# Kernel tuning notes

Measured on AMD Instinct MI355X. Metric: run time of the kernel, lower is better.

The kernel has to match this reference:

```python
import jax, jax.numpy as jnp
import numpy as np

TEMPERATURE = 12.5   # args.temperature (DeepEMD default)
EPS = 0.05           # entropic regularization for the OT (EMD) solve
N_ITERS = 100        # Sinkhorn iterations
COS_EPS = 1e-8       # F.cosine_similarity eps


def setup_inputs() -> dict:
    key = jax.random.key(0)
    k1, k2 = jax.random.split(key)
    B, C, H, W = 512, 1024, 8, 8
    proto = jax.random.normal(k1, (B, C, H, W), dtype=jnp.float32)
    query = jax.random.normal(k2, (B, C, H, W), dtype=jnp.float32)
    return {"proto": proto, "query": query}


def get_weight_vector(A, Bmap):
    """A,[b,c,h,w]; pooled Bmap reweights A's channels -> node weights [b, h*w]."""
    pooled = Bmap.mean(axis=(2, 3), keepdims=True)          # adaptive_avg_pool2d -> [b,c,1,1]
    comb = (A * pooled).sum(axis=1).reshape(A.shape[0], -1)  # [b, h*w]
    return jax.nn.relu(comb) + 0.001


def center(x):
    # args.norm == 'center': subtract channel mean
    return x - x.mean(axis=1, keepdims=True)


def cosine_sim_map(proto, query):
    """sim[b, q_node, p_node] = cosine similarity between flattened spatial nodes."""
    B, C = proto.shape[0], proto.shape[1]
    p = proto.reshape(B, C, -1).transpose(0, 2, 1)   # [b, Np, c]
    q = query.reshape(B, C, -1).transpose(0, 2, 1)   # [b, Nq, c]
    pn = p / jnp.maximum(jnp.linalg.norm(p, axis=-1, keepdims=True), COS_EPS)
    qn = q / jnp.maximum(jnp.linalg.norm(q, axis=-1, keepdims=True), COS_EPS)
    return jnp.einsum('bqc,bpc->bqp', qn, pn)        # [b, Nq, Np]


def sinkhorn_flow(cost, r, c):
    """Entropic-regularized OT flow with marginals r [b,N], c [b,M]; cost [b,N,M]."""
    K = jnp.exp(-cost / EPS)
    v0 = jnp.ones_like(c)

    def body(v, _):
        u = r / jnp.maximum(jnp.einsum('bnm,bm->bn', K, v), 1e-30)
        v = c / jnp.maximum(jnp.einsum('bnm,bn->bm', K, u), 1e-30)
        return v, None

    v, _ = jax.lax.scan(body, v0, None, length=N_ITERS)
    u = r / jnp.maximum(jnp.einsum('bnm,bm->bn', K, v), 1e-30)
    return u[:, :, None] * K * v[:, None, :]         # [b, N, M]


def reference(proto, query):
    # emd_forward(proto, query)
    weight_1 = get_weight_vector(query, proto)       # [b, Nq]
    weight_2 = get_weight_vector(proto, query)       # [b, Np]
    p = center(proto)
    q = center(query)
    sim = cosine_sim_map(p, q)                       # [b, Nq, Np]
    # get_emd_distance: solve OT on cost = 1 - sim with (normalized) node weights
    r = weight_1 / weight_1.sum(axis=-1, keepdims=True)
    c = weight_2 / weight_2.sum(axis=-1, keepdims=True)
    flow = sinkhorn_flow(1.0 - sim, r, c)
    num_node = weight_1.shape[-1]
    logits = (sim * flow).sum(axis=(-1, -2)) * (TEMPERATURE / num_node)
    return logits
```

## Files before the change

### kernel.cpp

```cpp
#include <hip/hip_runtime.h>
#include <math.h>

#define NCH    1024
#define NN     64
#define CK     32
#define KSC    28.853900817779268f
#define SPLIT  4
#define WSB    4352

#define STAT_Q(v) { sqp[0]+=(v).x; q2p[0]=fmaf((v).x,(v).x,q2p[0]); \
                    sqp[1]+=(v).y; q2p[1]=fmaf((v).y,(v).y,q2p[1]); \
                    sqp[2]+=(v).z; q2p[2]=fmaf((v).z,(v).z,q2p[2]); \
                    sqp[3]+=(v).w; q2p[3]=fmaf((v).w,(v).w,q2p[3]); }
#define STAT_P(v) { spp[0]+=(v).x; p2p[0]=fmaf((v).x,(v).x,p2p[0]); \
                    spp[1]+=(v).y; p2p[1]=fmaf((v).y,(v).y,p2p[1]); \
                    spp[2]+=(v).z; p2p[2]=fmaf((v).z,(v).z,p2p[2]); \
                    spp[3]+=(v).w; p2p[3]=fmaf((v).w,(v).w,p2p[3]); }

#define GRAM_CHUNK_BODY(NCHUNK_, QB_, PB_)                                     \
    for (int ch = 0; ch < (NCHUNK_); ++ch) {                                   \
        if (ch) __syncthreads();                                               \
        *(float4*)&stage[       ofs] = qv0;                                    \
        *(float4*)&stage[1024 + ofs] = qv1;                                    \
        *(float4*)&stage[2048 + ofs] = pv0;                                    \
        *(float4*)&stage[3072 + ofs] = pv1;                                    \
        float4 nq0, nq1, np0, np1;                                             \
        const bool more = (ch + 1 < (NCHUNK_));                                \
        if (more) {                                                            \
            const float* qn = (QB_) + (ch + 1) * 2048;                         \
            const float* pn = (PB_) + (ch + 1) * 2048;                         \
            nq0 = *(const float4*)(qn + ofs);                                  \
            nq1 = *(const float4*)(qn + 1024 + ofs);                           \
            np0 = *(const float4*)(pn + ofs);                                  \
            np1 = *(const float4*)(pn + 1024 + ofs);                           \
        }                                                                      \
        STAT_Q(qv0); STAT_Q(qv1);                                              \
        STAT_P(pv0); STAT_P(pv1);                                              \
        __syncthreads();                                                       \
        _Pragma("unroll 8")                                                    \
        for (int cc = 0; cc < CK; ++cc) {                                      \
            float4 a  = *(const float4*)&stage[cc * 64 + n0];                  \
            float4 bb = *(const float4*)&stage[2048 + cc * 64 + m0];           \
            acc[0][0]=fmaf(a.x,bb.x,acc[0][0]); acc[0][1]=fmaf(a.x,bb.y,acc[0][1]); \
            acc[0][2]=fmaf(a.x,bb.z,acc[0][2]); acc[0][3]=fmaf(a.x,bb.w,acc[0][3]); \
            acc[1][0]=fmaf(a.y,bb.x,acc[1][0]); acc[1][1]=fmaf(a.y,bb.y,acc[1][1]); \
            acc[1][2]=fmaf(a.y,bb.z,acc[1][2]); acc[1][3]=fmaf(a.y,bb.w,acc[1][3]); \
            acc[2][0]=fmaf(a.z,bb.x,acc[2][0]); acc[2][1]=fmaf(a.z,bb.y,acc[2][1]); \
            acc[2][2]=fmaf(a.z,bb.z,acc[2][2]); acc[2][3]=fmaf(a.z,bb.w,acc[2][3]); \
            acc[3][0]=fmaf(a.w,bb.x,acc[3][0]); acc[3][1]=fmaf(a.w,bb.y,acc[3][1]); \
            acc[3][2]=fmaf(a.w,bb.z,acc[3][2]); acc[3][3]=fmaf(a.w,bb.w,acc[3][3]); \
        }                                                                      \
        if (more) { qv0 = nq0; qv1 = nq1; pv0 = np0; pv1 = np1; }              \
    }

#define DOT16(KK, ARR) ({ \
    float4 x0 = *(const float4*)&ARR[sp4*16 +  0]; \
    float4 x1 = *(const float4*)&ARR[sp4*16 +  4]; \
    float4 x2 = *(const float4*)&ARR[sp4*16 +  8]; \
    float4 x3 = *(const float4*)&ARR[sp4*16 + 12]; \
    float a0 = 0.0f, a1 = 0.0f; \
    a0=fmaf(KK[0],x0.x,a0);  a1=fmaf(KK[1],x0.y,a1); \
    a0=fmaf(KK[2],x0.z,a0);  a1=fmaf(KK[3],x0.w,a1); \
    a0=fmaf(KK[4],x1.x,a0);  a1=fmaf(KK[5],x1.y,a1); \
    a0=fmaf(KK[6],x1.z,a0);  a1=fmaf(KK[7],x1.w,a1); \
    a0=fmaf(KK[8],x2.x,a0);  a1=fmaf(KK[9],x2.y,a1); \
    a0=fmaf(KK[10],x2.z,a0); a1=fmaf(KK[11],x2.w,a1); \
    a0=fmaf(KK[12],x3.x,a0); a1=fmaf(KK[13],x3.y,a1); \
    a0=fmaf(KK[14],x3.z,a0); a1=fmaf(KK[15],x3.w,a1); \
    a0 + a1; })

__global__ __launch_bounds__(256)
void gram_partial(const float* __restrict__ proto,
                  const float* __restrict__ query,
                  float* __restrict__ ws)
{
    __shared__ __align__(16) float stage[4096];

    const int bid = blockIdx.x;
    const int b = bid >> 2, s = bid & (SPLIT - 1);
    const int t  = threadIdx.x;
    const int tr = t >> 4, tc = t & 15;
    const int n0 = tr * 4, m0 = tc * 4;
    const int ofs = 4 * t;

    const float* __restrict__ pb = proto + (size_t)b * (NCH * NN) + s * (NCH / SPLIT) * NN;
    const float* __restrict__ qb = query + (size_t)b * (NCH * NN) + s * (NCH / SPLIT) * NN;

    float acc[4][4];
    #pragma unroll
    for (int i = 0; i < 4; ++i)
        #pragma unroll
        for (int j = 0; j < 4; ++j) acc[i][j] = 0.0f;
    float sqp[4] = {0,0,0,0}, q2p[4] = {0,0,0,0};
    float spp[4] = {0,0,0,0}, p2p[4] = {0,0,0,0};

    float4 qv0 = *(const float4*)(qb + ofs);
    float4 qv1 = *(const float4*)(qb + 1024 + ofs);
    float4 pv0 = *(const float4*)(pb + ofs);
    float4 pv1 = *(const float4*)(pb + 1024 + ofs);

    GRAM_CHUNK_BODY(NCH / SPLIT / CK, qb, pb)
    __syncthreads();

    float* __restrict__ wsb = ws + (size_t)bid * WSB;
    #pragma unroll
    for (int i = 0; i < 4; ++i) {
        float4 v; v.x = acc[i][0]; v.y = acc[i][1]; v.z = acc[i][2]; v.w = acc[i][3];
        *(float4*)&wsb[(n0 + i) * 64 + m0] = v;
    }

    #pragma unroll
    for (int k = 0; k < 4; ++k) {
        stage[t*16 +      k] = sqp[k];
        stage[t*16 +  4 + k] = q2p[k];
        stage[t*16 +  8 + k] = spp[k];
        stage[t*16 + 12 + k] = p2p[k];
    }
    __syncthreads();
    if (t < NN) {
        const int g = t >> 2, k = t & 3;
        float ssq = 0, sq2 = 0, ssp = 0, sp2 = 0;
        #pragma unroll
        for (int j = 0; j < 16; ++j) {
            const float* row = &stage[(j * 16 + g) * 16];
            ssq += row[k]; sq2 += row[4 + k]; ssp += row[8 + k]; sp2 += row[12 + k];
        }
        wsb[4096 +   0 + t] = ssq;
        wsb[4096 +  64 + t] = sq2;
        wsb[4096 + 128 + t] = ssp;
        wsb[4096 + 192 + t] = sp2;
    }
}

__global__ __launch_bounds__(256)
void emd_solve(const float* __restrict__ ws, float* __restrict__ out)
{
    __shared__ __align__(16) float stage[16 * 64];
    __shared__ __align__(16) float Kl [NN][68];
    __shared__ __align__(16) float KTl[NN][68];
    __shared__ __align__(16) float statL[4][NN];
    __shared__ __align__(16) float uL[NN];
    __shared__ __align__(16) float vL[NN];
    __shared__ __align__(16) float rL[NN];
    __shared__ __align__(16) float cL[NN];
    __shared__ float redl[4];

    const int b  = blockIdx.x;
    const int t  = threadIdx.x;
    const int tr = t >> 4, tc = t & 15;
    const int n0 = tr * 4, m0 = tc * 4;

    const float* __restrict__ wsb = ws + (size_t)b * SPLIT * WSB;

    float acc[4][4];
    #pragma unroll
    for (int i = 0; i < 4; ++i)
        #pragma unroll
        for (int j = 0; j < 4; ++j) acc[i][j] = 0.0f;
    #pragma unroll
    for (int s = 0; s < SPLIT; ++s) {
        const float* __restrict__ g = wsb + s * WSB;
        #pragma unroll
        for (int i = 0; i < 4; ++i) {
            float4 v = *(const float4*)&g[(n0 + i) * 64 + m0];
            acc[i][0] += v.x; acc[i][1] += v.y; acc[i][2] += v.z; acc[i][3] += v.w;
        }
    }
    if (t < NN) {
        float s0 = 0, s1 = 0, s2 = 0, s3 = 0;
        #pragma unroll
        for (int s = 0; s < SPLIT; ++s) {
            const float* __restrict__ g = wsb + s * WSB + 4096;
            s0 += g[t]; s1 += g[64 + t]; s2 += g[128 + t]; s3 += g[192 + t];
        }
        statL[0][t] = s0; statL[1][t] = s1; statL[2][t] = s2; statL[3][t] = s3;
    }
    #pragma unroll
    for (int i = 0; i < 4; ++i) {
        float s = acc[i][0] + acc[i][1] + acc[i][2] + acc[i][3];
        s += __shfl_xor(s, 1, 64); s += __shfl_xor(s, 2, 64);
        s += __shfl_xor(s, 4, 64); s += __shfl_xor(s, 8, 64);
        if (tc == 0) uL[n0 + i] = s;
    }
    #pragma unroll
    for (int j = 0; j < 4; ++j)
        stage[tr * 64 + m0 + j] = acc[0][j] + acc[1][j] + acc[2][j] + acc[3][j];
    __syncthreads();

    if (t < NN) {
        float cs = 0;
        #pragma unroll
        for (int i = 0; i < 16; ++i) cs += stage[i * 64 + t];
        float w2 = fmaxf(cs * (1.0f/64.0f), 0.0f) + 0.001f;
        float w1 = fmaxf(uL[t] * (1.0f/64.0f), 0.0f) + 0.001f;
        float s1 = w1, s2 = w2;
        #pragma unroll
        for (int m = 1; m < 64; m <<= 1) {
            s1 += __shfl_xor(s1, m, 64);
            s2 += __shfl_xor(s2, m, 64);
        }
        rL[t] = w1 / s1;
        cL[t] = w2 / s2;
        vL[t] = 1.0f;
    }
    {
        float nq_[4], np_[4], sqn[4], spm[4];
        #pragma unroll
        for (int i = 0; i < 4; ++i) {
            float sv  = statL[0][n0 + i];
            float var = statL[1][n0 + i] - sv * sv * (1.0f/1024.0f);
            nq_[i] = fmaxf(sqrtf(fmaxf(var, 0.0f)), 1e-8f);
            sqn[i] = sv;
        }
        #pragma unroll
        for (int j = 0; j < 4; ++j) {
            float sv  = statL[2][m0 + j];
            float var = statL[3][m0 + j] - sv * sv * (1.0f/1024.0f);
            np_[j] = fmaxf(sqrtf(fmaxf(var, 0.0f)), 1e-8f);
            spm[j] = sv;
        }
        #pragma unroll
        for (int i = 0; i < 4; ++i) {
            #pragma unroll
            for (int j = 0; j < 4; ++j) {
                float sim = (acc[i][j] - sqn[i] * spm[j] * (1.0f/1024.0f)) / (nq_[i] * np_[j]);
                acc[i][j] = sim;
                float Kv = exp2f((sim - 1.0f) * KSC);
                Kl [n0 + i][m0 + j] = Kv;
                KTl[m0 + j][n0 + i] = Kv;
            }
        }
    }
    __syncthreads();

    const int sn  = t >> 2;
    const int sp4 = t & 3;
    float Kr[16], KTr[16];
    #pragma unroll
    for (int jj = 0; jj < 4; ++jj) {
        float4 kv = *(const float4*)&Kl [sn][sp4 * 16 + jj * 4];
        float4 kt = *(const float4*)&KTl[sn][sp4 * 16 + jj * 4];
        Kr [jj*4+0]=kv.x; Kr [jj*4+1]=kv.y; Kr [jj*4+2]=kv.z; Kr [jj*4+3]=kv.w;
        KTr[jj*4+0]=kt.x; KTr[jj*4+1]=kt.y; KTr[jj*4+2]=kt.z; KTr[jj*4+3]=kt.w;
    }
    const float rreg = rL[sn];
    const float creg = cL[sn];

    for (int it = 0; it < 100; ++it) {
        float s = DOT16(Kr, vL);
        s += __shfl_xor(s, 1, 64); s += __shfl_xor(s, 2, 64);
        float u = rreg / fmaxf(s, 1e-30f);
        if (sp4 == 0) uL[sn] = u;
        __syncthreads();
        float s2 = DOT16(KTr, uL);
        s2 += __shfl_xor(s2, 1, 64); s2 += __shfl_xor(s2, 2, 64);
        float vv = creg / fmaxf(s2, 1e-30f);
        if (sp4 == 0) vL[sn] = vv;
        __syncthreads();
    }
    {
        float s = DOT16(Kr, vL);
        s += __shfl_xor(s, 1, 64); s += __shfl_xor(s, 2, 64);
        float u = rreg / fmaxf(s, 1e-30f);
        if (sp4 == 0) uL[sn] = u;
    }
    __syncthreads();

    float uu[4], vv_[4];
    #pragma unroll
    for (int i = 0; i < 4; ++i) uu[i]  = uL[n0 + i];
    #pragma unroll
    for (int j = 0; j < 4; ++j) vv_[j] = vL[m0 + j];
    float part = 0.0f;
    #pragma unroll
    for (int i = 0; i < 4; ++i) {
        #pragma unroll
        for (int j = 0; j < 4; ++j) {
            float sim = acc[i][j];
            float Kv  = exp2f((sim - 1.0f) * KSC);
            part = fmaf(sim * Kv, uu[i] * vv_[j], part);
        }
    }
    #pragma unroll
    for (int m = 1; m < 64; m <<= 1) part += __shfl_xor(part, m, 64);
    if ((t & 63) == 0) redl[t >> 6] = part;
    __syncthreads();
    if (t == 0) out[b] = (redl[0] + redl[1] + redl[2] + redl[3]) * (12.5f / 64.0f);
}

__global__ __launch_bounds__(256)
void deepemd_fused(const float* __restrict__ proto,
                   const float* __restrict__ query,
                   float* __restrict__ out)
{
    __shared__ __align__(16) float stage[2 * CK * NN];
    __shared__ __align__(16) float Kl [NN][68];
    __shared__ __align__(16) float KTl[NN][68];
    __shared__ __align__(16) float statL[4][NN];
    __shared__ __align__(16) float uL[NN];
    __shared__ __align__(16) float vL[NN];
    __shared__ __align__(16) float rL[NN];
    __shared__ __align__(16) float cL[NN];
    __shared__ float redl[4];

    const int b  = blockIdx.x;
    const int t  = threadIdx.x;
    const int tr = t >> 4, tc = t & 15;
    const int n0 = tr * 4, m0 = tc * 4;
    const int ofs = 4 * t;

    const float* __restrict__ pb = proto + (size_t)b * (NCH * NN);
    const float* __restrict__ qb = query + (size_t)b * (NCH * NN);

    float acc[4][4];
    #pragma unroll
    for (int i = 0; i < 4; ++i)
        #pragma unroll
        for (int j = 0; j < 4; ++j) acc[i][j] = 0.0f;
    float sqp[4] = {0,0,0,0}, q2p[4] = {0,0,0,0};
    float spp[4] = {0,0,0,0}, p2p[4] = {0,0,0,0};

    float4 qv0 = *(const float4*)(qb + ofs);
    float4 qv1 = *(const float4*)(qb + 1024 + ofs);
    float4 pv0 = *(const float4*)(pb + ofs);
    float4 pv1 = *(const float4*)(pb + 1024 + ofs);

    GRAM_CHUNK_BODY(NCH / CK, qb, pb)
    __syncthreads();

    #pragma unroll
    for (int i = 0; i < 4; ++i) {
        float s = acc[i][0] + acc[i][1] + acc[i][2] + acc[i][3];
        s += __shfl_xor(s, 1, 64); s += __shfl_xor(s, 2, 64);
        s += __shfl_xor(s, 4, 64); s += __shfl_xor(s, 8, 64);
        if (tc == 0) uL[n0 + i] = s;
    }
    #pragma unroll
    for (int k = 0; k < 4; ++k) {
        stage[t*16 +      k] = sqp[k];
        stage[t*16 +  4 + k] = q2p[k];
        stage[t*16 +  8 + k] = spp[k];
        stage[t*16 + 12 + k] = p2p[k];
    }
    __syncthreads();
    if (t < NN) {
        const int g = t >> 2, k = t & 3;
        float ssq = 0, sq2 = 0, ssp = 0, sp2 = 0;
        #pragma unroll
        for (int j = 0; j < 16; ++j) {
            const float* row = &stage[(j * 16 + g) * 16];
            ssq += row[k]; sq2 += row[4 + k]; ssp += row[8 + k]; sp2 += row[12 + k];
        }
        statL[0][t] = ssq; statL[1][t] = sq2; statL[2][t] = ssp; statL[3][t] = sp2;
    }
    __syncthreads();
    #pragma unroll
    for (int j = 0; j < 4; ++j)
        stage[tr * 64 + m0 + j] = acc[0][j] + acc[1][j] + acc[2][j] + acc[3][j];
    __syncthreads();
    if (t < NN) {
        float cs = 0;
        #pragma unroll
        for (int i = 0; i < 16; ++i) cs += stage[i * 64 + t];
        float w2 = fmaxf(cs * (1.0f/64.0f), 0.0f) + 0.001f;
        float w1 = fmaxf(uL[t] * (1.0f/64.0f), 0.0f) + 0.001f;
        float s1 = w1, s2 = w2;
        #pragma unroll
        for (int m = 1; m < 64; m <<= 1) {
            s1 += __shfl_xor(s1, m, 64);
            s2 += __shfl_xor(s2, m, 64);
        }
        rL[t] = w1 / s1;
        cL[t] = w2 / s2;
        vL[t] = 1.0f;
    }
    __syncthreads();

    {
        float nq_[4], np_[4], sqn[4], spm[4];
        #pragma unroll
        for (int i = 0; i < 4; ++i) {
            float sv  = statL[0][n0 + i];
            float var = statL[1][n0 + i] - sv * sv * (1.0f/1024.0f);
            nq_[i] = fmaxf(sqrtf(fmaxf(var, 0.0f)), 1e-8f);
            sqn[i] = sv;
        }
        #pragma unroll
        for (int j = 0; j < 4; ++j) {
            float sv  = statL[2][m0 + j];
            float var = statL[3][m0 + j] - sv * sv * (1.0f/1024.0f);
            np_[j] = fmaxf(sqrtf(fmaxf(var, 0.0f)), 1e-8f);
            spm[j] = sv;
        }
        #pragma unroll
        for (int i = 0; i < 4; ++i) {
            #pragma unroll
            for (int j = 0; j < 4; ++j) {
                float sim = (acc[i][j] - sqn[i] * spm[j] * (1.0f/1024.0f)) / (nq_[i] * np_[j]);
                acc[i][j] = sim;
                float Kv = exp2f((sim - 1.0f) * KSC);
                Kl [n0 + i][m0 + j] = Kv;
                KTl[m0 + j][n0 + i] = Kv;
            }
        }
    }
    __syncthreads();

    const int sn  = t >> 2;
    const int sp4 = t & 3;
    float Kr[16], KTr[16];
    #pragma unroll
    for (int jj = 0; jj < 4; ++jj) {
        float4 kv = *(const float4*)&Kl [sn][sp4 * 16 + jj * 4];
        float4 kt = *(const float4*)&KTl[sn][sp4 * 16 + jj * 4];
        Kr [jj*4+0]=kv.x; Kr [jj*4+1]=kv.y; Kr [jj*4+2]=kv.z; Kr [jj*4+3]=kv.w;
        KTr[jj*4+0]=kt.x; KTr[jj*4+1]=kt.y; KTr[jj*4+2]=kt.z; KTr[jj*4+3]=kt.w;
    }
    const float rreg = rL[sn];
    const float creg = cL[sn];

    for (int it = 0; it < 100; ++it) {
        float s = DOT16(Kr, vL);
        s += __shfl_xor(s, 1, 64); s += __shfl_xor(s, 2, 64);
        float u = rreg / fmaxf(s, 1e-30f);
        if (sp4 == 0) uL[sn] = u;
        __syncthreads();
        float s2 = DOT16(KTr, uL);
        s2 += __shfl_xor(s2, 1, 64); s2 += __shfl_xor(s2, 2, 64);
        float vv = creg / fmaxf(s2, 1e-30f);
        if (sp4 == 0) vL[sn] = vv;
        __syncthreads();
    }
    {
        float s = DOT16(Kr, vL);
        s += __shfl_xor(s, 1, 64); s += __shfl_xor(s, 2, 64);
        float u = rreg / fmaxf(s, 1e-30f);
        if (sp4 == 0) uL[sn] = u;
    }
    __syncthreads();

    float uu[4], vv_[4];
    #pragma unroll
    for (int i = 0; i < 4; ++i) uu[i]  = uL[n0 + i];
    #pragma unroll
    for (int j = 0; j < 4; ++j) vv_[j] = vL[m0 + j];
    float part = 0.0f;
    #pragma unroll
    for (int i = 0; i < 4; ++i) {
        #pragma unroll
        for (int j = 0; j < 4; ++j) {
            float sim = acc[i][j];
            float Kv  = exp2f((sim - 1.0f) * KSC);
            part = fmaf(sim * Kv, uu[i] * vv_[j], part);
        }
    }
    #pragma unroll
    for (int m = 1; m < 64; m <<= 1) part += __shfl_xor(part, m, 64);
    if ((t & 63) == 0) redl[t >> 6] = part;
    __syncthreads();
    if (t == 0) out[b] = (redl[0] + redl[1] + redl[2] + redl[3]) * (12.5f / 64.0f);
}

extern "C" void kernel_launch(void* const* d_in, const int* in_sizes, int n_in,
                              void* d_out, int out_size, void* d_ws, size_t ws_size,
                              hipStream_t stream) {
    const float* proto = (const float*)d_in[0];
    const float* query = (const float*)d_in[1];
    float* out = (float*)d_out;
    (void)in_sizes; (void)n_in; (void)out_size;

    const size_t need = (size_t)512 * SPLIT * WSB * sizeof(float);
    if (ws_size >= need) {
        gram_partial<<<dim3(512 * SPLIT), dim3(256), 0, stream>>>(proto, query, (float*)d_ws);
        emd_solve  <<<dim3(512),         dim3(256), 0, stream>>>((const float*)d_ws, out);
    } else {
        deepemd_fused<<<dim3(512), dim3(256), 0, stream>>>(proto, query, out);
    }
}
```

Measured before the change: 134.5 us.

## Rewrite gram kernel with 8x8 register tiles and per-wave channel split

Replaces the 256-thread Gram partial kernel with a 128-thread version. Each of the two waves handles half the channel slice, each thread computes an 8x8 output tile, and every wave has its own double-buffered LDS stage, so there are no block-wide barriers inside the loop. Per-wave partial Gram matrices and column statistics are combined through LDS at the end. This raises arithmetic intensity per LDS load and removes barrier stalls, at the cost of more registers (launch bounds 128,3), fewer threads per block, and an extra cross-wave reduction. emd_solve is only moved within the file and is unchanged.

```diff
diff --git a/kernel.cpp b/kernel.cpp
--- a/kernel.cpp
+++ b/kernel.cpp
@@ -7,6 +7,8 @@
 #define KSC    28.853900817779268f
 #define SPLIT  4
 #define WSB    4352
+#define CHUNK_CH 8
+#define NCHUNKS  16
 
 #define STAT_Q(v) { sqp[0]+=(v).x; q2p[0]=fmaf((v).x,(v).x,q2p[0]); \
                     sqp[1]+=(v).y; q2p[1]=fmaf((v).y,(v).y,q2p[1]); \
@@ -16,6 +18,303 @@
                     spp[1]+=(v).y; p2p[1]=fmaf((v).y,(v).y,p2p[1]); \
                     spp[2]+=(v).z; p2p[2]=fmaf((v).z,(v).z,p2p[2]); \
                     spp[3]+=(v).w; p2p[3]=fmaf((v).w,(v).w,p2p[3]); }
+
+__global__ __launch_bounds__(128, 3)
+void gram_partial2(const float* __restrict__ proto,
+                   const float* __restrict__ query,
+                   float* __restrict__ ws)
+{
+    __shared__ __align__(16) float smem[4096];
+    __shared__ __align__(16) float statd[4][NN];
+
+    const int bid = blockIdx.x;
+    const int b = bid >> 2, s = bid & 3;
+    const int t = threadIdx.x;
+    const int w = t >> 6;
+    const int l = t & 63;
+    const int r0 = (l >> 3) * 8;
+    const int c0 = (l & 7) * 8;
+    const int o1 = 4 * l;
+    const int o2 = 256 + 4 * l;
+
+    const float* __restrict__ qw = query + (size_t)b * (NCH * NN) + (s * 256 + w * 128) * NN;
+    const float* __restrict__ pw = proto + (size_t)b * (NCH * NN) + (s * 256 + w * 128) * NN;
+
+    float* const stg = &smem[w * 2048];
+
+    float acc[8][8];
+    #pragma unroll
+    for (int i = 0; i < 8; ++i)
+        #pragma unroll
+        for (int j = 0; j < 8; ++j) acc[i][j] = 0.0f;
+    float sqp[4] = {0,0,0,0}, q2p[4] = {0,0,0,0};
+    float spp[4] = {0,0,0,0}, p2p[4] = {0,0,0,0};
+
+    float4 qv0 = *(const float4*)(qw + o1);
+    float4 qv1 = *(const float4*)(qw + o2);
+    float4 pv0 = *(const float4*)(pw + o1);
+    float4 pv1 = *(const float4*)(pw + o2);
+
+    for (int ch = 0; ch < NCHUNKS; ++ch) {
+        float* const sq = stg + (ch & 1) * 1024;
+        float* const sp = sq + 512;
+        *(float4*)(sq + o1) = qv0;
+        *(float4*)(sq + o2) = qv1;
+        *(float4*)(sp + o1) = pv0;
+        *(float4*)(sp + o2) = pv1;
+
+        STAT_Q(qv0); STAT_Q(qv1);
+        STAT_P(pv0); STAT_P(pv1);
+
+        if (ch + 1 < NCHUNKS) {
+            const float* qn = qw + (ch + 1) * 512;
+            const float* pn = pw + (ch + 1) * 512;
+            qv0 = *(const float4*)(qn + o1);
+            qv1 = *(const float4*)(qn + o2);
+            pv0 = *(const float4*)(pn + o1);
+            pv1 = *(const float4*)(pn + o2);
+        }
+
+        #pragma unroll
+        for (int cc = 0; cc < CHUNK_CH; ++cc) {
+            float4 a0 = *(const float4*)(sq + cc * 64 + r0);
+            float4 a1 = *(const float4*)(sq + cc * 64 + r0 + 4);
+            float4 b0 = *(const float4*)(sp + cc * 64 + c0);
+            float4 b1 = *(const float4*)(sp + cc * 64 + c0 + 4);
+            const float av[8] = {a0.x,a0.y,a0.z,a0.w,a1.x,a1.y,a1.z,a1.w};
+            const float bv[8] = {b0.x,b0.y,b0.z,b0.w,b1.x,b1.y,b1.z,b1.w};
+            #pragma unroll
+            for (int i = 0; i < 8; ++i)
+                #pragma unroll
+                for (int j = 0; j < 8; ++j)
+                    acc[i][j] = fmaf(av[i], bv[j], acc[i][j]);
+        }
+    }
+
+    #pragma unroll
+    for (int k = 0; k < 4; ++k) {
+        sqp[k] += __shfl_xor(sqp[k], 16, 64); sqp[k] += __shfl_xor(sqp[k], 32, 64);
+        q2p[k] += __shfl_xor(q2p[k], 16, 64); q2p[k] += __shfl_xor(q2p[k], 32, 64);
+        spp[k] += __shfl_xor(spp[k], 16, 64); spp[k] += __shfl_xor(spp[k], 32, 64);
+        p2p[k] += __shfl_xor(p2p[k], 16, 64); p2p[k] += __shfl_xor(p2p[k], 32, 64);
+    }
+
+    __syncthreads();
+
+    if (w == 0) {
+        #pragma unroll
+        for (int i = 0; i < 8; ++i) {
+            float4 v0; v0.x=acc[i][0]; v0.y=acc[i][1]; v0.z=acc[i][2]; v0.w=acc[i][3];
+            float4 v1; v1.x=acc[i][4]; v1.y=acc[i][5]; v1.z=acc[i][6]; v1.w=acc[i][7];
+            *(float4*)&smem[(r0 + i) * 64 + c0]     = v0;
+            *(float4*)&smem[(r0 + i) * 64 + c0 + 4] = v1;
+        }
+        if (l < 16) {
+            #pragma unroll
+            for (int k = 0; k < 4; ++k) {
+                statd[0][4*l+k] = sqp[k];
+                statd[1][4*l+k] = q2p[k];
+                statd[2][4*l+k] = spp[k];
+                statd[3][4*l+k] = p2p[k];
+            }
+        }
+    }
+    __syncthreads();
+
+    if (w == 1) {
+        float* __restrict__ wsb = ws + (size_t)bid * WSB;
+        #pragma unroll
+        for (int i = 0; i < 8; ++i) {
+            float4 d0 = *(const float4*)&smem[(r0 + i) * 64 + c0];
+            float4 d1 = *(const float4*)&smem[(r0 + i) * 64 + c0 + 4];
+            float4 v0; v0.x=acc[i][0]+d0.x; v0.y=acc[i][1]+d0.y; v0.z=acc[i][2]+d0.z; v0.w=acc[i][3]+d0.w;
+            float4 v1; v1.x=acc[i][4]+d1.x; v1.y=acc[i][5]+d1.y; v1.z=acc[i][6]+d1.z; v1.w=acc[i][7]+d1.w;
+            *(float4*)&wsb[(r0 + i) * 64 + c0]     = v0;
+            *(float4*)&wsb[(r0 + i) * 64 + c0 + 4] = v1;
+        }
+        if (l < 16) {
+            #pragma unroll
+            for (int k = 0; k < 4; ++k) {
+                wsb[4096 +   0 + 4*l+k] = statd[0][4*l+k] + sqp[k];
+                wsb[4096 +  64 + 4*l+k] = statd[1][4*l+k] + q2p[k];
+                wsb[4096 + 128 + 4*l+k] = statd[2][4*l+k] + spp[k];
+                wsb[4096 + 192 + 4*l+k] = statd[3][4*l+k] + p2p[k];
+            }
+        }
+    }
+}
+
+#define DOT16(KK, ARR) ({ \
+    float4 x0 = *(const float4*)&ARR[sp4*16 +  0]; \
+    float4 x1 = *(const float4*)&ARR[sp4*16 +  4]; \
+    float4 x2 = *(const float4*)&ARR[sp4*16 +  8]; \
+    float4 x3 = *(const float4*)&ARR[sp4*16 + 12]; \
+    float a0 = 0.0f, a1 = 0.0f; \
+    a0=fmaf(KK[0],x0.x,a0);  a1=fmaf(KK[1],x0.y,a1); \
+    a0=fmaf(KK[2],x0.z,a0);  a1=fmaf(KK[3],x0.w,a1); \
+    a0=fmaf(KK[4],x1.x,a0);  a1=fmaf(KK[5],x1.y,a1); \
+    a0=fmaf(KK[6],x1.z,a0);  a1=fmaf(KK[7],x1.w,a1); \
+    a0=fmaf(KK[8],x2.x,a0);  a1=fmaf(KK[9],x2.y,a1); \
+    a0=fmaf(KK[10],x2.z,a0); a1=fmaf(KK[11],x2.w,a1); \
+    a0=fmaf(KK[12],x3.x,a0); a1=fmaf(KK[13],x3.y,a1); \
+    a0=fmaf(KK[14],x3.z,a0); a1=fmaf(KK[15],x3.w,a1); \
+    a0 + a1; })
+
+__global__ __launch_bounds__(256)
+void emd_solve(const float* __restrict__ ws, float* __restrict__ out)
+{
+    __shared__ __align__(16) float stage[16 * 64];
+    __shared__ __align__(16) float Kl [NN][68];
+    __shared__ __align__(16) float KTl[NN][68];
+    __shared__ __align__(16) float statL[4][NN];
+    __shared__ __align__(16) float uL[NN];
+    __shared__ __align__(16) float vL[NN];
+    __shared__ __align__(16) float rL[NN];
+    __shared__ __align__(16) float cL[NN];
+    __shared__ float redl[4];
+
+    const int b  = blockIdx.x;
+    const int t  = threadIdx.x;
+    const int tr = t >> 4, tc = t & 15;
+    const int n0 = tr * 4, m0 = tc * 4;
+
+    const float* __restrict__ wsb = ws + (size_t)b * SPLIT * WSB;
+
+    float acc[4][4];
+    #pragma unroll
+    for (int i = 0; i < 4; ++i)
+        #pragma unroll
+        for (int j = 0; j < 4; ++j) acc[i][j] = 0.0f;
+    #pragma unroll
+    for (int s = 0; s < SPLIT; ++s) {
+        const float* __restrict__ g = wsb + s * WSB;
+        #pragma unroll
+        for (int i = 0; i < 4; ++i) {
+            float4 v = *(const float4*)&g[(n0 + i) * 64 + m0];
+            acc[i][0] += v.x; acc[i][1] += v.y; acc[i][2] += v.z; acc[i][3] += v.w;
+        }
+    }
+    if (t < NN) {
+        float s0 = 0, s1 = 0, s2 = 0, s3 = 0;
+        #pragma unroll
+        for (int s = 0; s < SPLIT; ++s) {
+            const float* __restrict__ g = wsb + s * WSB + 4096;
+            s0 += g[t]; s1 += g[64 + t]; s2 += g[128 + t]; s3 += g[192 + t];
+        }
+        statL[0][t] = s0; statL[1][t] = s1; statL[2][t] = s2; statL[3][t] = s3;
+    }
+    #pragma unroll
+    for (int i = 0; i < 4; ++i) {
+        float s = acc[i][0] + acc[i][1] + acc[i][2] + acc[i][3];
+        s += __shfl_xor(s, 1, 64); s += __shfl_xor(s, 2, 64);
+        s += __shfl_xor(s, 4, 64); s += __shfl_xor(s, 8, 64);
+        if (tc == 0) uL[n0 + i] = s;
+    }
+    #pragma unroll
+    for (int j = 0; j < 4; ++j)
+        stage[tr * 64 + m0 + j] = acc[0][j] + acc[1][j] + acc[2][j] + acc[3][j];
+    __syncthreads();
+
+    if (t < NN) {
+        float cs = 0;
+        #pragma unroll
+        for (int i = 0; i < 16; ++i) cs += stage[i * 64 + t];
+        float w2 = fmaxf(cs * (1.0f/64.0f), 0.0f) + 0.001f;
+        float w1 = fmaxf(uL[t] * (1.0f/64.0f), 0.0f) + 0.001f;
+        float s1 = w1, s2 = w2;
+        #pragma unroll
+        for (int m = 1; m < 64; m <<= 1) {
+            s1 += __shfl_xor(s1, m, 64);
+            s2 += __shfl_xor(s2, m, 64);
+        }
+        rL[t] = w1 / s1;
+        cL[t] = w2 / s2;
+        vL[t] = 1.0f;
+    }
+    {
+        float nq_[4], np_[4], sqn[4], spm[4];
+        #pragma unroll
+        for (int i = 0; i < 4; ++i) {
+            float sv  = statL[0][n0 + i];
+            float var = statL[1][n0 + i] - sv * sv * (1.0f/1024.0f);
+            nq_[i] = fmaxf(sqrtf(fmaxf(var, 0.0f)), 1e-8f);
+            sqn[i] = sv;
+        }
+        #pragma unroll
+        for (int j = 0; j < 4; ++j) {
+            float sv  = statL[2][m0 + j];
+            float var = statL[3][m0 + j] - sv * sv * (1.0f/1024.0f);
+            np_[j] = fmaxf(sqrtf(fmaxf(var, 0.0f)), 1e-8f);
+            spm[j] = sv;
+        }
+        #pragma unroll
+        for (int i = 0; i < 4; ++i) {
+            #pragma unroll
+            for (int j = 0; j < 4; ++j) {
+                float sim = (acc[i][j] - sqn[i] * spm[j] * (1.0f/1024.0f)) / (nq_[i] * np_[j]);
+                acc[i][j] = sim;
+                float Kv = exp2f((sim - 1.0f) * KSC);
+                Kl [n0 + i][m0 + j] = Kv;
+                KTl[m0 + j][n0 + i] = Kv;
+            }
+        }
+    }
+    __syncthreads();
+
+    const int sn  = t >> 2;
+    const int sp4 = t & 3;
+    float Kr[16], KTr[16];
+    #pragma unroll
+    for (int jj = 0; jj < 4; ++jj) {
+        float4 kv = *(const float4*)&Kl [sn][sp4 * 16 + jj * 4];
+        float4 kt = *(const float4*)&KTl[sn][sp4 * 16 + jj * 4];
+        Kr [jj*4+0]=kv.x; Kr [jj*4+1]=kv.y; Kr [jj*4+2]=kv.z; Kr [jj*4+3]=kv.w;
+        KTr[jj*4+0]=kt.x; KTr[jj*4+1]=kt.y; KTr[jj*4+2]=kt.z; KTr[jj*4+3]=kt.w;
+    }
+    const float rreg = rL[sn];
+    const float creg = cL[sn];
+
+    for (int it = 0; it < 100; ++it) {
+        float s = DOT16(Kr, vL);
+        s += __shfl_xor(s, 1, 64); s += __shfl_xor(s, 2, 64);
+        float u = rreg / fmaxf(s, 1e-30f);
+        if (sp4 == 0) uL[sn] = u;
+        __syncthreads();
+        float s2 = DOT16(KTr, uL);
+        s2 += __shfl_xor(s2, 1, 64); s2 += __shfl_xor(s2, 2, 64);
+        float vv = creg / fmaxf(s2, 1e-30f);
+        if (sp4 == 0) vL[sn] = vv;
+        __syncthreads();
+    }
+    {
+        float s = DOT16(Kr, vL);
+        s += __shfl_xor(s, 1, 64); s += __shfl_xor(s, 2, 64);
+        float u = rreg / fmaxf(s, 1e-30f);
+        if (sp4 == 0) uL[sn] = u;
+    }
+    __syncthreads();
+
+    float uu[4], vv_[4];
+    #pragma unroll
+    for (int i = 0; i < 4; ++i) uu[i]  = uL[n0 + i];
+    #pragma unroll
+    for (int j = 0; j < 4; ++j) vv_[j] = vL[m0 + j];
+    float part = 0.0f;
+    #pragma unroll
+    for (int i = 0; i < 4; ++i) {
+        #pragma unroll
+        for (int j = 0; j < 4; ++j) {
+            float sim = acc[i][j];
+            float Kv  = exp2f((sim - 1.0f) * KSC);
+            part = fmaf(sim * Kv, uu[i] * vv_[j], part);
+        }
+    }
+    #pragma unroll
+    for (int m = 1; m < 64; m <<= 1) part += __shfl_xor(part, m, 64);
+    if ((t & 63) == 0) redl[t >> 6] = part;
+    __syncthreads();
+    if (t == 0) out[b] = (redl[0] + redl[1] + redl[2] + redl[3]) * (12.5f / 64.0f);
+}
 
 #define GRAM_CHUNK_BODY(NCHUNK_, QB_, PB_)                                     \
     for (int ch = 0; ch < (NCHUNK_); ++ch) {                                   \
@@ -53,241 +352,6 @@
         if (more) { qv0 = nq0; qv1 = nq1; pv0 = np0; pv1 = np1; }              \
     }
 
-#define DOT16(KK, ARR) ({ \
-    float4 x0 = *(const float4*)&ARR[sp4*16 +  0]; \
-    float4 x1 = *(const float4*)&ARR[sp4*16 +  4]; \
-    float4 x2 = *(const float4*)&ARR[sp4*16 +  8]; \
-    float4 x3 = *(const float4*)&ARR[sp4*16 + 12]; \
-    float a0 = 0.0f, a1 = 0.0f; \
-    a0=fmaf(KK[0],x0.x,a0);  a1=fmaf(KK[1],x0.y,a1); \
-    a0=fmaf(KK[2],x0.z,a0);  a1=fmaf(KK[3],x0.w,a1); \
-    a0=fmaf(KK[4],x1.x,a0);  a1=fmaf(KK[5],x1.y,a1); \
-    a0=fmaf(KK[6],x1.z,a0);  a1=fmaf(KK[7],x1.w,a1); \
-    a0=fmaf(KK[8],x2.x,a0);  a1=fmaf(KK[9],x2.y,a1); \
-    a0=fmaf(KK[10],x2.z,a0); a1=fmaf(KK[11],x2.w,a1); \
-    a0=fmaf(KK[12],x3.x,a0); a1=fmaf(KK[13],x3.y,a1); \
-    a0=fmaf(KK[14],x3.z,a0); a1=fmaf(KK[15],x3.w,a1); \
-    a0 + a1; })
-
-__global__ __launch_bounds__(256)
-void gram_partial(const float* __restrict__ proto,
-                  const float* __restrict__ query,
-                  float* __restrict__ ws)
-{
-    __shared__ __align__(16) float stage[4096];
-
-    const int bid = blockIdx.x;
-    const int b = bid >> 2, s = bid & (SPLIT - 1);
-    const int t  = threadIdx.x;
-    const int tr = t >> 4, tc = t & 15;
-    const int n0 = tr * 4, m0 = tc * 4;
-    const int ofs = 4 * t;
-
-    const float* __restrict__ pb = proto + (size_t)b * (NCH * NN) + s * (NCH / SPLIT) * NN;
-    const float* __restrict__ qb = query + (size_t)b * (NCH * NN) + s * (NCH / SPLIT) * NN;
-
-    float acc[4][4];
-    #pragma unroll
-    for (int i = 0; i < 4; ++i)
-        #pragma unroll
-        for (int j = 0; j < 4; ++j) acc[i][j] = 0.0f;
-    float sqp[4] = {0,0,0,0}, q2p[4] = {0,0,0,0};
-    float spp[4] = {0,0,0,0}, p2p[4] = {0,0,0,0};
-
-    float4 qv0 = *(const float4*)(qb + ofs);
-    float4 qv1 = *(const float4*)(qb + 1024 + ofs);
-    float4 pv0 = *(const float4*)(pb + ofs);
-    float4 pv1 = *(const float4*)(pb + 1024 + ofs);
-
-    GRAM_CHUNK_BODY(NCH / SPLIT / CK, qb, pb)
-    __syncthreads();
-
-    float* __restrict__ wsb = ws + (size_t)bid * WSB;
-    #pragma unroll
-    for (int i = 0; i < 4; ++i) {
-        float4 v; v.x = acc[i][0]; v.y = acc[i][1]; v.z = acc[i][2]; v.w = acc[i][3];
-        *(float4*)&wsb[(n0 + i) * 64 + m0] = v;
-    }
-
-    #pragma unroll
-    for (int k = 0; k < 4; ++k) {
-        stage[t*16 +      k] = sqp[k];
-        stage[t*16 +  4 + k] = q2p[k];
-        stage[t*16 +  8 + k] = spp[k];
-        stage[t*16 + 12 + k] = p2p[k];
-    }
-    __syncthreads();
-    if (t < NN) {
-        const int g = t >> 2, k = t & 3;
-        float ssq = 0, sq2 = 0, ssp = 0, sp2 = 0;
-        #pragma unroll
-        for (int j = 0; j < 16; ++j) {
-            const float* row = &stage[(j * 16 + g) * 16];
-            ssq += row[k]; sq2 += row[4 + k]; ssp += row[8 + k]; sp2 += row[12 + k];
-        }
-        wsb[4096 +   0 + t] = ssq;
-        wsb[4096 +  64 + t] = sq2;
-        wsb[4096 + 128 + t] = ssp;
-        wsb[4096 + 192 + t] = sp2;
-    }
-}
-
-__global__ __launch_bounds__(256)
-void emd_solve(const float* __restrict__ ws, float* __restrict__ out)
-{
-    __shared__ __align__(16) float stage[16 * 64];
-    __shared__ __align__(16) float Kl [NN][68];
-    __shared__ __align__(16) float KTl[NN][68];
-    __shared__ __align__(16) float statL[4][NN];
-    __shared__ __align__(16) float uL[NN];
-    __shared__ __align__(16) float vL[NN];
-    __shared__ __align__(16) float rL[NN];
-    __shared__ __align__(16) float cL[NN];
-    __shared__ float redl[4];
-
-    const int b  = blockIdx.x;
-    const int t  = threadIdx.x;
-    const int tr = t >> 4, tc = t & 15;
-    const int n0 = tr * 4, m0 = tc * 4;
-
-    const float* __restrict__ wsb = ws + (size_t)b * SPLIT * WSB;
-
-    float acc[4][4];
-    #pragma unroll
-    for (int i = 0; i < 4; ++i)
-        #pragma unroll
-        for (int j = 0; j < 4; ++j) acc[i][j] = 0.0f;
-    #pragma unroll
-    for (int s = 0; s < SPLIT; ++s) {
-        const float* __restrict__ g = wsb + s * WSB;
-        #pragma unroll
-        for (int i = 0; i < 4; ++i) {
-            float4 v = *(const float4*)&g[(n0 + i) * 64 + m0];
-            acc[i][0] += v.x; acc[i][1] += v.y; acc[i][2] += v.z; acc[i][3] += v.w;
-        }
-    }
-    if (t < NN) {
-        float s0 = 0, s1 = 0, s2 = 0, s3 = 0;
-        #pragma unroll
-        for (int s = 0; s < SPLIT; ++s) {
-            const float* __restrict__ g = wsb + s * WSB + 4096;
-            s0 += g[t]; s1 += g[64 + t]; s2 += g[128 + t]; s3 += g[192 + t];
-        }
-        statL[0][t] = s0; statL[1][t] = s1; statL[2][t] = s2; statL[3][t] = s3;
-    }
-    #pragma unroll
-    for (int i = 0; i < 4; ++i) {
-        float s = acc[i][0] + acc[i][1] + acc[i][2] + acc[i][3];
-        s += __shfl_xor(s, 1, 64); s += __shfl_xor(s, 2, 64);
-        s += __shfl_xor(s, 4, 64); s += __shfl_xor(s, 8, 64);
-        if (tc == 0) uL[n0 + i] = s;
-    }
-    #pragma unroll
-    for (int j = 0; j < 4; ++j)
-        stage[tr * 64 + m0 + j] = acc[0][j] + acc[1][j] + acc[2][j] + acc[3][j];
-    __syncthreads();
-
-    if (t < NN) {
-        float cs = 0;
-        #pragma unroll
-        for (int i = 0; i < 16; ++i) cs += stage[i * 64 + t];
-        float w2 = fmaxf(cs * (1.0f/64.0f), 0.0f) + 0.001f;
-        float w1 = fmaxf(uL[t] * (1.0f/64.0f), 0.0f) + 0.001f;
-        float s1 = w1, s2 = w2;
-        #pragma unroll
-        for (int m = 1; m < 64; m <<= 1) {
-            s1 += __shfl_xor(s1, m, 64);
-            s2 += __shfl_xor(s2, m, 64);
-        }
-        rL[t] = w1 / s1;
-        cL[t] = w2 / s2;
-        vL[t] = 1.0f;
-    }
-    {
-        float nq_[4], np_[4], sqn[4], spm[4];
-        #pragma unroll
-        for (int i = 0; i < 4; ++i) {
-            float sv  = statL[0][n0 + i];
-            float var = statL[1][n0 + i] - sv * sv * (1.0f/1024.0f);
-            nq_[i] = fmaxf(sqrtf(fmaxf(var, 0.0f)), 1e-8f);
-            sqn[i] = sv;
-        }
-        #pragma unroll
-        for (int j = 0; j < 4; ++j) {
-            float sv  = statL[2][m0 + j];
-            float var = statL[3][m0 + j] - sv * sv * (1.0f/1024.0f);
-            np_[j] = fmaxf(sqrtf(fmaxf(var, 0.0f)), 1e-8f);
-            spm[j] = sv;
-        }
-        #pragma unroll
-        for (int i = 0; i < 4; ++i) {
-            #pragma unroll
-            for (int j = 0; j < 4; ++j) {
-                float sim = (acc[i][j] - sqn[i] * spm[j] * (1.0f/1024.0f)) / (nq_[i] * np_[j]);
-                acc[i][j] = sim;
-                float Kv = exp2f((sim - 1.0f) * KSC);
-                Kl [n0 + i][m0 + j] = Kv;
-                KTl[m0 + j][n0 + i] = Kv;
-            }
-        }
-    }
-    __syncthreads();
-
-    const int sn  = t >> 2;
-    const int sp4 = t & 3;
-    float Kr[16], KTr[16];
-    #pragma unroll
-    for (int jj = 0; jj < 4; ++jj) {
-        float4 kv = *(const float4*)&Kl [sn][sp4 * 16 + jj * 4];
-        float4 kt = *(const float4*)&KTl[sn][sp4 * 16 + jj * 4];
-        Kr [jj*4+0]=kv.x; Kr [jj*4+1]=kv.y; Kr [jj*4+2]=kv.z; Kr [jj*4+3]=kv.w;
-        KTr[jj*4+0]=kt.x; KTr[jj*4+1]=kt.y; KTr[jj*4+2]=kt.z; KTr[jj*4+3]=kt.w;
-    }
-    const float rreg = rL[sn];
-    const float creg = cL[sn];
-
-    for (int it = 0; it < 100; ++it) {
-        float s = DOT16(Kr, vL);
-        s += __shfl_xor(s, 1, 64); s += __shfl_xor(s, 2, 64);
-        float u = rreg / fmaxf(s, 1e-30f);
-        if (sp4 == 0) uL[sn] = u;
-        __syncthreads();
-        float s2 = DOT16(KTr, uL);
-        s2 += __shfl_xor(s2, 1, 64); s2 += __shfl_xor(s2, 2, 64);
-        float vv = creg / fmaxf(s2, 1e-30f);
-        if (sp4 == 0) vL[sn] = vv;
-        __syncthreads();
-    }
-    {
-        float s = DOT16(Kr, vL);
-        s += __shfl_xor(s, 1, 64); s += __shfl_xor(s, 2, 64);
-        float u = rreg / fmaxf(s, 1e-30f);
-        if (sp4 == 0) uL[sn] = u;
-    }
-    __syncthreads();
-
-    float uu[4], vv_[4];
-    #pragma unroll
-    for (int i = 0; i < 4; ++i) uu[i]  = uL[n0 + i];
-    #pragma unroll
-    for (int j = 0; j < 4; ++j) vv_[j] = vL[m0 + j];
-    float part = 0.0f;
-    #pragma unroll
-    for (int i = 0; i < 4; ++i) {
-        #pragma unroll
-        for (int j = 0; j < 4; ++j) {
-            float sim = acc[i][j];
-            float Kv  = exp2f((sim - 1.0f) * KSC);
-            part = fmaf(sim * Kv, uu[i] * vv_[j], part);
-        }
-    }
-    #pragma unroll
-    for (int m = 1; m < 64; m <<= 1) part += __shfl_xor(part, m, 64);
-    if ((t & 63) == 0) redl[t >> 6] = part;
-    __syncthreads();
-    if (t == 0) out[b] = (redl[0] + redl[1] + redl[2] + redl[3]) * (12.5f / 64.0f);
-}
-
 __global__ __launch_bounds__(256)
 void deepemd_fused(const float* __restrict__ proto,
                    const float* __restrict__ query,
@@ -471,8 +535,8 @@
 
     const size_t need = (size_t)512 * SPLIT * WSB * sizeof(float);
     if (ws_size >= need) {
-        gram_partial<<<dim3(512 * SPLIT), dim3(256), 0, stream>>>(proto, query, (float*)d_ws);
-        emd_solve  <<<dim3(512),         dim3(256), 0, stream>>>((const float*)d_ws, out);
+        gram_partial2<<<dim3(512 * SPLIT), dim3(128), 0, stream>>>(proto, query, (float*)d_ws);
+        emd_solve    <<<dim3(512),         dim3(256), 0, stream>>>((const float*)d_ws, out);
     } else {
         deepemd_fused<<<dim3(512), dim3(256), 0, stream>>>(proto, query, out);
     }
```

Result: no change. 131.9 us (-1.9%).
